# Optimization experiments

Measured on AMD Instinct MI355X. Metric: run time of the kernel, lower is better.

## Reference

```python
import jax, jax.numpy as jnp
import numpy as np

S, B, H, I, E = 512, 2, 1024, 2816, 8  # seq_len, batch, hidden, intermediate, num_local_experts


def setup_inputs() -> dict:
    key = jax.random.key(0)
    ks = jax.random.split(key, 5)
    return {
        "hidden_states": jax.random.normal(ks[0], (S, B, H), dtype=jnp.float32),
        "router_w": jax.random.normal(ks[1], (E, H), dtype=jnp.float32) * 0.02,
        "gate_w": jax.random.normal(ks[2], (E, I, H), dtype=jnp.float32) * 0.02,
        "up_w": jax.random.normal(ks[3], (E, I, H), dtype=jnp.float32) * 0.02,
        "down_w": jax.random.normal(ks[4], (E, H, I), dtype=jnp.float32) * 0.02,
    }


def reference(hidden_states, router_w, gate_w, up_w, down_w):
    # Router: linear hidden -> num_experts, top-1 routing (num_experts_per_tok == 1).
    router_logits = jnp.einsum('sbh,eh->sbe', hidden_states, router_w)  # [S,B,E]
    routing_indices = jnp.argmax(router_logits, axis=-1)  # [S,B], top-1 == argmax
    # NOTE: the source computes routing_weights = sigmoid(top logit) but never
    # applies it in _combine_expert_outputs; we faithfully omit the scaling.

    out = jnp.zeros_like(hidden_states)
    for e in range(E):  # fixed small expert count; masked dense dispatch/combine
        mask = (routing_indices == e)[..., None]  # [S,B,1]
        xe = jnp.where(mask, hidden_states, 0.0)
        g = jnp.einsum('sbh,ih->sbi', xe, gate_w[e])
        u = jnp.einsum('sbh,ih->sbi', xe, up_w[e])
        ye = jnp.einsum('sbi,hi->sbh', jax.nn.silu(g) * u, down_w[e])
        out = out + jnp.where(mask, ye, 0.0)
    return out
```

## Files before the change

kernel.cpp:

```cpp
#include <hip/hip_runtime.h>
#include <math.h>

constexpr int H_ = 1024;
constexpr int I_ = 2816;
constexpr int E_ = 8;
constexpr int T_ = 1024;

typedef __bf16 bf16x8 __attribute__((ext_vector_type(8)));
typedef float f32x4 __attribute__((ext_vector_type(4)));

__device__ __forceinline__ ushort f2bf(float f) {
    uint32_t u = __float_as_uint(f);
    u += 0x7fff + ((u >> 16) & 1);
    return (ushort)(u >> 16);
}
__device__ __forceinline__ uint pack2(float lo, float hi) {
    return (uint)f2bf(lo) | ((uint)f2bf(hi) << 16);
}


__global__ __launch_bounds__(64) void router_kernel(const float* __restrict__ hidden,
                                                    const float* __restrict__ rw,
                                                    int* __restrict__ counts,
                                                    int* __restrict__ tlist,
                                                    ushort* __restrict__ xbf) {
    const int t = blockIdx.x;
    const int lane = threadIdx.x;
    const float* x = hidden + (size_t)t * H_ + lane * 16;
    float4 v[4];
#pragma unroll
    for (int j = 0; j < 4; j++) v[j] = ((const float4*)x)[j];
    uint2* xb = (uint2*)(xbf + (size_t)t * H_ + lane * 16);
#pragma unroll
    for (int j = 0; j < 4; j++) xb[j] = make_uint2(pack2(v[j].x, v[j].y), pack2(v[j].z, v[j].w));
    float acc[E_];
#pragma unroll
    for (int e = 0; e < E_; e++) {
        const float4* r = (const float4*)(rw + e * H_ + lane * 16);
        float a = 0.f;
#pragma unroll
        for (int j = 0; j < 4; j++) {
            float4 rv = r[j];
            a += v[j].x * rv.x + v[j].y * rv.y + v[j].z * rv.z + v[j].w * rv.w;
        }
        acc[e] = a;
    }
#pragma unroll
    for (int e = 0; e < E_; e++) {
#pragma unroll
        for (int off = 32; off >= 1; off >>= 1)
            acc[e] += __shfl_xor(acc[e], off, 64);
    }
    if (lane == 0) {
        int best = 0;
        float bv = acc[0];
#pragma unroll
        for (int e = 1; e < E_; e++) {
            if (acc[e] > bv) { bv = acc[e]; best = e; }
        }
        int pos = atomicAdd(&counts[best], 1);
        tlist[best * T_ + pos] = t;
    }
}

__global__ __launch_bounds__(256, 3) void gateup_kernel(const ushort* __restrict__ xbf,
                                                        const float* __restrict__ gate_w,
                                                        const float* __restrict__ up_w,
                                                        const int* __restrict__ counts,
                                                        const int* __restrict__ tlist,
                                                        ushort* __restrict__ act) {
    const int e  = blockIdx.y;
    const int i0 = blockIdx.x * 32;
    const int cnt = counts[e];
    const int tid = threadIdx.x;

    __shared__ ushort Xs[256 * 72];
    __shared__ ushort Gs[32 * 72];
    __shared__ ushort Us[32 * 72];
    __shared__ int toks[256];

    const int wv = tid >> 6, lane = tid & 63, quad = lane >> 4, l15 = lane & 15;
    const float* gw = gate_w + (size_t)e * I_ * H_ + (size_t)i0 * H_;
    const float* uw = up_w   + (size_t)e * I_ * H_ + (size_t)i0 * H_;

    for (int toff = 0; toff < cnt; toff += 256) {
        __syncthreads();
        {
            int p = toff + tid;
            toks[tid] = (p < cnt) ? tlist[e * T_ + p] : -1;
        }
        __syncthreads();
        int tokr[8];
#pragma unroll
        for (int p = 0; p < 8; p++) tokr[p] = toks[(tid + p * 256) >> 3];

        f32x4 accg[4][2], accu[4][2];
#pragma unroll
        for (int mi = 0; mi < 4; mi++)
#pragma unroll
            for (int nj = 0; nj < 2; nj++) {
                accg[mi][nj] = (f32x4){0.f, 0.f, 0.f, 0.f};
                accu[mi][nj] = (f32x4){0.f, 0.f, 0.f, 0.f};
            }

        uint4 xv[8];
        float4 gv[2], uv[2];
#pragma unroll
        for (int p = 0; p < 8; p++) {
            int idx = tid + p * 256;
            xv[p] = (tokr[p] >= 0)
                ? *(const uint4*)(xbf + (size_t)tokr[p] * H_ + ((idx & 7) << 3))
                : make_uint4(0u, 0u, 0u, 0u);
        }
#pragma unroll
        for (int p = 0; p < 2; p++) {
            int idx = tid + p * 256;
            int row = idx >> 4, c4 = (idx & 15) << 2;
            gv[p] = *(const float4*)(gw + (size_t)row * H_ + c4);
            uv[p] = *(const float4*)(uw + (size_t)row * H_ + c4);
        }

        for (int k0 = 0; k0 < H_; k0 += 64) {
            __syncthreads();
#pragma unroll
            for (int p = 0; p < 8; p++) {
                int idx = tid + p * 256;
                *(uint4*)&Xs[(idx >> 3) * 72 + ((idx & 7) << 3)] = xv[p];
            }
#pragma unroll
            for (int p = 0; p < 2; p++) {
                int idx = tid + p * 256;
                int row = idx >> 4, c4 = (idx & 15) << 2;
                *(uint2*)&Gs[row * 72 + c4] = make_uint2(pack2(gv[p].x, gv[p].y), pack2(gv[p].z, gv[p].w));
                *(uint2*)&Us[row * 72 + c4] = make_uint2(pack2(uv[p].x, uv[p].y), pack2(uv[p].z, uv[p].w));
            }
            if (k0 + 64 < H_) {
                int kn = k0 + 64;
#pragma unroll
                for (int p = 0; p < 8; p++) {
                    int idx = tid + p * 256;
                    xv[p] = (tokr[p] >= 0)
                        ? *(const uint4*)(xbf + (size_t)tokr[p] * H_ + kn + ((idx & 7) << 3))
                        : make_uint4(0u, 0u, 0u, 0u);
                }
#pragma unroll
                for (int p = 0; p < 2; p++) {
                    int idx = tid + p * 256;
                    int row = idx >> 4, c4 = (idx & 15) << 2;
                    gv[p] = *(const float4*)(gw + (size_t)row * H_ + kn + c4);
                    uv[p] = *(const float4*)(uw + (size_t)row * H_ + kn + c4);
                }
            }
            __syncthreads();
#pragma unroll
            for (int kk = 0; kk < 64; kk += 32) {
                const int kb = kk + quad * 8;
                bf16x8 bg[2], bu[2], a[4];
#pragma unroll
                for (int nj = 0; nj < 2; nj++) {
                    bg[nj] = *(const bf16x8*)&Gs[(nj * 16 + l15) * 72 + kb];
                    bu[nj] = *(const bf16x8*)&Us[(nj * 16 + l15) * 72 + kb];
                }
#pragma unroll
                for (int mi = 0; mi < 4; mi++)
                    a[mi] = *(const bf16x8*)&Xs[(wv * 64 + mi * 16 + l15) * 72 + kb];
#pragma unroll
                for (int mi = 0; mi < 4; mi++)
#pragma unroll
                    for (int nj = 0; nj < 2; nj++) {
                        accg[mi][nj] = __builtin_amdgcn_mfma_f32_16x16x32_bf16(a[mi], bg[nj], accg[mi][nj], 0, 0, 0);
                        accu[mi][nj] = __builtin_amdgcn_mfma_f32_16x16x32_bf16(a[mi], bu[nj], accu[mi][nj], 0, 0, 0);
                    }
            }
        }

#pragma unroll
        for (int mi = 0; mi < 4; mi++)
#pragma unroll
            for (int r = 0; r < 4; r++) {
                int tok = toks[wv * 64 + mi * 16 + quad * 4 + r];
                if (tok < 0) continue;
#pragma unroll
                for (int nj = 0; nj < 2; nj++) {
                    float g = accg[mi][nj][r], u = accu[mi][nj][r];
                    float s = g / (1.f + __expf(-g)) * u;
                    act[(size_t)tok * I_ + i0 + nj * 16 + l15] = f2bf(s);
                }
            }
    }
}

__global__ __launch_bounds__(256, 3) void down_kernel(const ushort* __restrict__ act,
                                                      const float* __restrict__ down_w,
                                                      const int* __restrict__ counts,
                                                      const int* __restrict__ tlist,
                                                      float* __restrict__ out) {
    const int e  = blockIdx.y;
    const int h0 = blockIdx.x * 32;
    const int cnt = counts[e];
    const int tid = threadIdx.x;

    __shared__ ushort As[256 * 72];
    __shared__ ushort Ds[32 * 72];
    __shared__ int toks[256];

    const int wv = tid >> 6, lane = tid & 63, quad = lane >> 4, l15 = lane & 15;
    const float* dw = down_w + (size_t)e * H_ * I_ + (size_t)h0 * I_;

    for (int toff = 0; toff < cnt; toff += 256) {
        __syncthreads();
        {
            int p = toff + tid;
            toks[tid] = (p < cnt) ? tlist[e * T_ + p] : -1;
        }
        __syncthreads();
        int tokr[8];
#pragma unroll
        for (int p = 0; p < 8; p++) tokr[p] = toks[(tid + p * 256) >> 3];

        f32x4 acc[4][2];
#pragma unroll
        for (int mi = 0; mi < 4; mi++)
#pragma unroll
            for (int nj = 0; nj < 2; nj++) acc[mi][nj] = (f32x4){0.f, 0.f, 0.f, 0.f};

        uint4 av[8];
        float4 dv[2];
#pragma unroll
        for (int p = 0; p < 8; p++) {
            int idx = tid + p * 256;
            av[p] = (tokr[p] >= 0)
                ? *(const uint4*)(act + (size_t)tokr[p] * I_ + ((idx & 7) << 3))
                : make_uint4(0u, 0u, 0u, 0u);
        }
#pragma unroll
        for (int p = 0; p < 2; p++) {
            int idx = tid + p * 256;
            int row = idx >> 4, c4 = (idx & 15) << 2;
            dv[p] = *(const float4*)(dw + (size_t)row * I_ + c4);
        }

        for (int k0 = 0; k0 < I_; k0 += 64) {
            __syncthreads();
#pragma unroll
            for (int p = 0; p < 8; p++) {
                int idx = tid + p * 256;
                *(uint4*)&As[(idx >> 3) * 72 + ((idx & 7) << 3)] = av[p];
            }
#pragma unroll
            for (int p = 0; p < 2; p++) {
                int idx = tid + p * 256;
                int row = idx >> 4, c4 = (idx & 15) << 2;
                *(uint2*)&Ds[row * 72 + c4] = make_uint2(pack2(dv[p].x, dv[p].y), pack2(dv[p].z, dv[p].w));
            }
            if (k0 + 64 < I_) {
                int kn = k0 + 64;
#pragma unroll
                for (int p = 0; p < 8; p++) {
                    int idx = tid + p * 256;
                    av[p] = (tokr[p] >= 0)
                        ? *(const uint4*)(act + (size_t)tokr[p] * I_ + kn + ((idx & 7) << 3))
                        : make_uint4(0u, 0u, 0u, 0u);
                }
#pragma unroll
                for (int p = 0; p < 2; p++) {
                    int idx = tid + p * 256;
                    int row = idx >> 4, c4 = (idx & 15) << 2;
                    dv[p] = *(const float4*)(dw + (size_t)row * I_ + kn + c4);
                }
            }
            __syncthreads();
#pragma unroll
            for (int kk = 0; kk < 64; kk += 32) {
                const int kb = kk + quad * 8;
                bf16x8 b[2], a[4];
#pragma unroll
                for (int nj = 0; nj < 2; nj++)
                    b[nj] = *(const bf16x8*)&Ds[(nj * 16 + l15) * 72 + kb];
#pragma unroll
                for (int mi = 0; mi < 4; mi++)
                    a[mi] = *(const bf16x8*)&As[(wv * 64 + mi * 16 + l15) * 72 + kb];
#pragma unroll
                for (int mi = 0; mi < 4; mi++)
#pragma unroll
                    for (int nj = 0; nj < 2; nj++)
                        acc[mi][nj] = __builtin_amdgcn_mfma_f32_16x16x32_bf16(a[mi], b[nj], acc[mi][nj], 0, 0, 0);
            }
        }

#pragma unroll
        for (int mi = 0; mi < 4; mi++)
#pragma unroll
            for (int r = 0; r < 4; r++) {
                int tok = toks[wv * 64 + mi * 16 + quad * 4 + r];
                if (tok < 0) continue;
#pragma unroll
                for (int nj = 0; nj < 2; nj++)
                    out[(size_t)tok * H_ + h0 + nj * 16 + l15] = acc[mi][nj][r];
            }
    }
}

extern "C" void kernel_launch(void* const* d_in, const int* in_sizes, int n_in,
                              void* d_out, int out_size, void* d_ws, size_t ws_size,
                              hipStream_t stream) {
    const float* hidden = (const float*)d_in[0];
    const float* rw     = (const float*)d_in[1];
    const float* gate_w = (const float*)d_in[2];
    const float* up_w   = (const float*)d_in[3];
    const float* down_w = (const float*)d_in[4];
    float* out = (float*)d_out;

    int* counts = (int*)d_ws;
    int* tlist  = counts + E_;
    ushort* xbf = (ushort*)(tlist + E_ * T_);
    ushort* act = xbf + (size_t)T_ * H_;

    hipMemsetAsync(counts, 0, E_ * sizeof(int), stream);
    hipLaunchKernelGGL(router_kernel, dim3(T_), dim3(64), 0, stream, hidden, rw, counts, tlist, xbf);
    hipLaunchKernelGGL(gateup_kernel, dim3(I_ / 32, E_), dim3(256), 0, stream,
                       xbf, gate_w, up_w, counts, tlist, act);
    hipLaunchKernelGGL(down_kernel, dim3(H_ / 32, E_), dim3(256), 0, stream,
                       act, down_w, counts, tlist, out);
}
```

Before: 392.7 us.

## Load MFMA operands directly from global into registers, drop LDS staging

Both expert GEMM kernels stop staging token and weight tiles in shared memory. Each lane now loads its MFMA fragment straight from global memory into registers and converts fp32 weights to bf16 in registers. A two-stage register double buffer with an unrolled k loop replaces the __syncthreads-based pipeline, and waves with no tokens now exit early. The down kernel's output tile shrinks to 16 columns with twice as many blocks, and launch bounds drop to 2 blocks per SM. This removes LDS traffic and barriers but loses cross-wave reuse, so each wave re-reads the weights and the gathered activation rows from global or cache.

```diff
diff --git a/kernel.cpp b/kernel.cpp
--- a/kernel.cpp
+++ b/kernel.cpp
@@ -16,6 +16,15 @@
 }
 __device__ __forceinline__ uint pack2(float lo, float hi) {
     return (uint)f2bf(lo) | ((uint)f2bf(hi) << 16);
+}
+__device__ __forceinline__ bf16x8 cvt8(float4 a, float4 b) {
+    union { uint u[4]; bf16x8 v; } r;
+    r.u[0] = pack2(a.x, a.y); r.u[1] = pack2(a.z, a.w);
+    r.u[2] = pack2(b.x, b.y); r.u[3] = pack2(b.z, b.w);
+    return r.v;
+}
+__device__ __forceinline__ bf16x8 as_bf16x8(uint4 v) {
+    union { uint4 u; bf16x8 b; } c; c.u = v; return c.b;
 }
 
 
@@ -63,7 +72,7 @@
     }
 }
 
-__global__ __launch_bounds__(256, 3) void gateup_kernel(const ushort* __restrict__ xbf,
+__global__ __launch_bounds__(256, 2) void gateup_kernel(const ushort* __restrict__ xbf,
                                                         const float* __restrict__ gate_w,
                                                         const float* __restrict__ up_w,
                                                         const int* __restrict__ counts,
@@ -73,26 +82,28 @@
     const int i0 = blockIdx.x * 32;
     const int cnt = counts[e];
     const int tid = threadIdx.x;
-
-    __shared__ ushort Xs[256 * 72];
-    __shared__ ushort Gs[32 * 72];
-    __shared__ ushort Us[32 * 72];
+    const int wv = tid >> 6, lane = tid & 63, quad = lane >> 4, l15 = lane & 15;
+
     __shared__ int toks[256];
 
-    const int wv = tid >> 6, lane = tid & 63, quad = lane >> 4, l15 = lane & 15;
-    const float* gw = gate_w + (size_t)e * I_ * H_ + (size_t)i0 * H_;
-    const float* uw = up_w   + (size_t)e * I_ * H_ + (size_t)i0 * H_;
+    const float* gw0 = gate_w + ((size_t)e * I_ + i0 + l15) * H_ + quad * 8;
+    const float* gw1 = gw0 + (size_t)16 * H_;
+    const float* uw0 = up_w   + ((size_t)e * I_ + i0 + l15) * H_ + quad * 8;
+    const float* uw1 = uw0 + (size_t)16 * H_;
 
     for (int toff = 0; toff < cnt; toff += 256) {
         __syncthreads();
-        {
-            int p = toff + tid;
-            toks[tid] = (p < cnt) ? tlist[e * T_ + p] : -1;
-        }
-        __syncthreads();
-        int tokr[8];
-#pragma unroll
-        for (int p = 0; p < 8; p++) tokr[p] = toks[(tid + p * 256) >> 3];
+        { int p = toff + tid; toks[tid] = (p < cnt) ? tlist[e * T_ + p] : -1; }
+        __syncthreads();
+        if (cnt - toff <= wv * 64) continue;
+
+        int tka[4];
+        const ushort* xa[4];
+#pragma unroll
+        for (int mi = 0; mi < 4; mi++) {
+            tka[mi] = toks[wv * 64 + mi * 16 + l15];
+            xa[mi] = xbf + (size_t)(tka[mi] < 0 ? 0 : tka[mi]) * H_ + quad * 8;
+        }
 
         f32x4 accg[4][2], accu[4][2];
 #pragma unroll
@@ -103,76 +114,49 @@
                 accu[mi][nj] = (f32x4){0.f, 0.f, 0.f, 0.f};
             }
 
-        uint4 xv[8];
-        float4 gv[2], uv[2];
-#pragma unroll
-        for (int p = 0; p < 8; p++) {
-            int idx = tid + p * 256;
-            xv[p] = (tokr[p] >= 0)
-                ? *(const uint4*)(xbf + (size_t)tokr[p] * H_ + ((idx & 7) << 3))
-                : make_uint4(0u, 0u, 0u, 0u);
-        }
-#pragma unroll
-        for (int p = 0; p < 2; p++) {
-            int idx = tid + p * 256;
-            int row = idx >> 4, c4 = (idx & 15) << 2;
-            gv[p] = *(const float4*)(gw + (size_t)row * H_ + c4);
-            uv[p] = *(const float4*)(uw + (size_t)row * H_ + c4);
-        }
-
+        uint4 a0[4], a1[4];
+        float4 g0[2][2], g1[2][2], u0[2][2], u1[2][2];
+
+#define GU_LOAD(A, G, U, kk) do {                                                   \
+        const int k_ = (kk);                                                        \
+        _Pragma("unroll")                                                           \
+        for (int mi = 0; mi < 4; mi++)                                              \
+            A[mi] = (tka[mi] >= 0) ? *(const uint4*)(xa[mi] + k_)                   \
+                                   : make_uint4(0u, 0u, 0u, 0u);                    \
+        G[0][0] = *(const float4*)(gw0 + k_); G[0][1] = *(const float4*)(gw0 + k_ + 4); \
+        G[1][0] = *(const float4*)(gw1 + k_); G[1][1] = *(const float4*)(gw1 + k_ + 4); \
+        U[0][0] = *(const float4*)(uw0 + k_); U[0][1] = *(const float4*)(uw0 + k_ + 4); \
+        U[1][0] = *(const float4*)(uw1 + k_); U[1][1] = *(const float4*)(uw1 + k_ + 4); \
+    } while (0)
+
+#define GU_MFMA(A, G, U) do {                                                       \
+        bf16x8 bg[2], bu[2];                                                        \
+        _Pragma("unroll")                                                           \
+        for (int nj = 0; nj < 2; nj++) {                                            \
+            bg[nj] = cvt8(G[nj][0], G[nj][1]);                                      \
+            bu[nj] = cvt8(U[nj][0], U[nj][1]);                                      \
+        }                                                                           \
+        _Pragma("unroll")                                                           \
+        for (int mi = 0; mi < 4; mi++) {                                            \
+            bf16x8 aa = as_bf16x8(A[mi]);                                           \
+            _Pragma("unroll")                                                       \
+            for (int nj = 0; nj < 2; nj++) {                                        \
+                accg[mi][nj] = __builtin_amdgcn_mfma_f32_16x16x32_bf16(aa, bg[nj], accg[mi][nj], 0, 0, 0); \
+                accu[mi][nj] = __builtin_amdgcn_mfma_f32_16x16x32_bf16(aa, bu[nj], accu[mi][nj], 0, 0, 0); \
+            }                                                                       \
+        }                                                                           \
+    } while (0)
+
+        GU_LOAD(a0, g0, u0, 0);
+#pragma unroll 1
         for (int k0 = 0; k0 < H_; k0 += 64) {
-            __syncthreads();
-#pragma unroll
-            for (int p = 0; p < 8; p++) {
-                int idx = tid + p * 256;
-                *(uint4*)&Xs[(idx >> 3) * 72 + ((idx & 7) << 3)] = xv[p];
-            }
-#pragma unroll
-            for (int p = 0; p < 2; p++) {
-                int idx = tid + p * 256;
-                int row = idx >> 4, c4 = (idx & 15) << 2;
-                *(uint2*)&Gs[row * 72 + c4] = make_uint2(pack2(gv[p].x, gv[p].y), pack2(gv[p].z, gv[p].w));
-                *(uint2*)&Us[row * 72 + c4] = make_uint2(pack2(uv[p].x, uv[p].y), pack2(uv[p].z, uv[p].w));
-            }
-            if (k0 + 64 < H_) {
-                int kn = k0 + 64;
-#pragma unroll
-                for (int p = 0; p < 8; p++) {
-                    int idx = tid + p * 256;
-                    xv[p] = (tokr[p] >= 0)
-                        ? *(const uint4*)(xbf + (size_t)tokr[p] * H_ + kn + ((idx & 7) << 3))
-                        : make_uint4(0u, 0u, 0u, 0u);
-                }
-#pragma unroll
-                for (int p = 0; p < 2; p++) {
-                    int idx = tid + p * 256;
-                    int row = idx >> 4, c4 = (idx & 15) << 2;
-                    gv[p] = *(const float4*)(gw + (size_t)row * H_ + kn + c4);
-                    uv[p] = *(const float4*)(uw + (size_t)row * H_ + kn + c4);
-                }
-            }
-            __syncthreads();
-#pragma unroll
-            for (int kk = 0; kk < 64; kk += 32) {
-                const int kb = kk + quad * 8;
-                bf16x8 bg[2], bu[2], a[4];
-#pragma unroll
-                for (int nj = 0; nj < 2; nj++) {
-                    bg[nj] = *(const bf16x8*)&Gs[(nj * 16 + l15) * 72 + kb];
-                    bu[nj] = *(const bf16x8*)&Us[(nj * 16 + l15) * 72 + kb];
-                }
-#pragma unroll
-                for (int mi = 0; mi < 4; mi++)
-                    a[mi] = *(const bf16x8*)&Xs[(wv * 64 + mi * 16 + l15) * 72 + kb];
-#pragma unroll
-                for (int mi = 0; mi < 4; mi++)
-#pragma unroll
-                    for (int nj = 0; nj < 2; nj++) {
-                        accg[mi][nj] = __builtin_amdgcn_mfma_f32_16x16x32_bf16(a[mi], bg[nj], accg[mi][nj], 0, 0, 0);
-                        accu[mi][nj] = __builtin_amdgcn_mfma_f32_16x16x32_bf16(a[mi], bu[nj], accu[mi][nj], 0, 0, 0);
-                    }
-            }
-        }
+            GU_LOAD(a1, g1, u1, k0 + 32);
+            GU_MFMA(a0, g0, u0);
+            if (k0 + 64 < H_) GU_LOAD(a0, g0, u0, k0 + 64);
+            GU_MFMA(a1, g1, u1);
+        }
+#undef GU_LOAD
+#undef GU_MFMA
 
 #pragma unroll
         for (int mi = 0; mi < 4; mi++)
@@ -190,103 +174,69 @@
     }
 }
 
-__global__ __launch_bounds__(256, 3) void down_kernel(const ushort* __restrict__ act,
+__global__ __launch_bounds__(256, 2) void down_kernel(const ushort* __restrict__ act,
                                                       const float* __restrict__ down_w,
                                                       const int* __restrict__ counts,
                                                       const int* __restrict__ tlist,
                                                       float* __restrict__ out) {
     const int e  = blockIdx.y;
-    const int h0 = blockIdx.x * 32;
+    const int h0 = blockIdx.x * 16;
     const int cnt = counts[e];
     const int tid = threadIdx.x;
-
-    __shared__ ushort As[256 * 72];
-    __shared__ ushort Ds[32 * 72];
+    const int wv = tid >> 6, lane = tid & 63, quad = lane >> 4, l15 = lane & 15;
+
     __shared__ int toks[256];
-
-    const int wv = tid >> 6, lane = tid & 63, quad = lane >> 4, l15 = lane & 15;
-    const float* dw = down_w + (size_t)e * H_ * I_ + (size_t)h0 * I_;
+    const float* dw = down_w + ((size_t)e * H_ + h0 + l15) * I_ + quad * 8;
 
     for (int toff = 0; toff < cnt; toff += 256) {
         __syncthreads();
-        {
-            int p = toff + tid;
-            toks[tid] = (p < cnt) ? tlist[e * T_ + p] : -1;
-        }
-        __syncthreads();
-        int tokr[8];
-#pragma unroll
-        for (int p = 0; p < 8; p++) tokr[p] = toks[(tid + p * 256) >> 3];
-
-        f32x4 acc[4][2];
-#pragma unroll
-        for (int mi = 0; mi < 4; mi++)
-#pragma unroll
-            for (int nj = 0; nj < 2; nj++) acc[mi][nj] = (f32x4){0.f, 0.f, 0.f, 0.f};
-
-        uint4 av[8];
-        float4 dv[2];
-#pragma unroll
-        for (int p = 0; p < 8; p++) {
-            int idx = tid + p * 256;
-            av[p] = (tokr[p] >= 0)
-                ? *(const uint4*)(act + (size_t)tokr[p] * I_ + ((idx & 7) << 3))
-                : make_uint4(0u, 0u, 0u, 0u);
-        }
-#pragma unroll
-        for (int p = 0; p < 2; p++) {
-            int idx = tid + p * 256;
-            int row = idx >> 4, c4 = (idx & 15) << 2;
-            dv[p] = *(const float4*)(dw + (size_t)row * I_ + c4);
-        }
-
+        { int p = toff + tid; toks[tid] = (p < cnt) ? tlist[e * T_ + p] : -1; }
+        __syncthreads();
+        if (cnt - toff <= wv * 64) continue;
+
+        int tka[4];
+        const ushort* xa[4];
+#pragma unroll
+        for (int mi = 0; mi < 4; mi++) {
+            tka[mi] = toks[wv * 64 + mi * 16 + l15];
+            xa[mi] = act + (size_t)(tka[mi] < 0 ? 0 : tka[mi]) * I_ + quad * 8;
+        }
+
+        f32x4 acc[4];
+#pragma unroll
+        for (int mi = 0; mi < 4; mi++) acc[mi] = (f32x4){0.f, 0.f, 0.f, 0.f};
+
+        uint4 a0[4], a1[4];
+        float4 d0[2], d1[2];
+
+#define DN_LOAD(A, D, kk) do {                                                      \
+        const int k_ = (kk);                                                        \
+        _Pragma("unroll")                                                           \
+        for (int mi = 0; mi < 4; mi++)                                              \
+            A[mi] = (tka[mi] >= 0) ? *(const uint4*)(xa[mi] + k_)                   \
+                                   : make_uint4(0u, 0u, 0u, 0u);                    \
+        D[0] = *(const float4*)(dw + k_); D[1] = *(const float4*)(dw + k_ + 4);     \
+    } while (0)
+
+#define DN_MFMA(A, D) do {                                                          \
+        bf16x8 bd = cvt8(D[0], D[1]);                                               \
+        _Pragma("unroll")                                                           \
+        for (int mi = 0; mi < 4; mi++) {                                            \
+            bf16x8 aa = as_bf16x8(A[mi]);                                           \
+            acc[mi] = __builtin_amdgcn_mfma_f32_16x16x32_bf16(aa, bd, acc[mi], 0, 0, 0); \
+        }                                                                           \
+    } while (0)
+
+        DN_LOAD(a0, d0, 0);
+#pragma unroll 1
         for (int k0 = 0; k0 < I_; k0 += 64) {
-            __syncthreads();
-#pragma unroll
-            for (int p = 0; p < 8; p++) {
-                int idx = tid + p * 256;
-                *(uint4*)&As[(idx >> 3) * 72 + ((idx & 7) << 3)] = av[p];
-            }
-#pragma unroll
-            for (int p = 0; p < 2; p++) {
-                int idx = tid + p * 256;
-                int row = idx >> 4, c4 = (idx & 15) << 2;
-                *(uint2*)&Ds[row * 72 + c4] = make_uint2(pack2(dv[p].x, dv[p].y), pack2(dv[p].z, dv[p].w));
-            }
-            if (k0 + 64 < I_) {
-                int kn = k0 + 64;
-#pragma unroll
-                for (int p = 0; p < 8; p++) {
-                    int idx = tid + p * 256;
-                    av[p] = (tokr[p] >= 0)
-                        ? *(const uint4*)(act + (size_t)tokr[p] * I_ + kn + ((idx & 7) << 3))
-                        : make_uint4(0u, 0u, 0u, 0u);
-                }
-#pragma unroll
-                for (int p = 0; p < 2; p++) {
-                    int idx = tid + p * 256;
-                    int row = idx >> 4, c4 = (idx & 15) << 2;
-                    dv[p] = *(const float4*)(dw + (size_t)row * I_ + kn + c4);
-                }
-            }
-            __syncthreads();
-#pragma unroll
-            for (int kk = 0; kk < 64; kk += 32) {
-                const int kb = kk + quad * 8;
-                bf16x8 b[2], a[4];
-#pragma unroll
-                for (int nj = 0; nj < 2; nj++)
-                    b[nj] = *(const bf16x8*)&Ds[(nj * 16 + l15) * 72 + kb];
-#pragma unroll
-                for (int mi = 0; mi < 4; mi++)
-                    a[mi] = *(const bf16x8*)&As[(wv * 64 + mi * 16 + l15) * 72 + kb];
-#pragma unroll
-                for (int mi = 0; mi < 4; mi++)
-#pragma unroll
-                    for (int nj = 0; nj < 2; nj++)
-                        acc[mi][nj] = __builtin_amdgcn_mfma_f32_16x16x32_bf16(a[mi], b[nj], acc[mi][nj], 0, 0, 0);
-            }
-        }
+            DN_LOAD(a1, d1, k0 + 32);
+            DN_MFMA(a0, d0);
+            if (k0 + 64 < I_) DN_LOAD(a0, d0, k0 + 64);
+            DN_MFMA(a1, d1);
+        }
+#undef DN_LOAD
+#undef DN_MFMA
 
 #pragma unroll
         for (int mi = 0; mi < 4; mi++)
@@ -294,9 +244,7 @@
             for (int r = 0; r < 4; r++) {
                 int tok = toks[wv * 64 + mi * 16 + quad * 4 + r];
                 if (tok < 0) continue;
-#pragma unroll
-                for (int nj = 0; nj < 2; nj++)
-                    out[(size_t)tok * H_ + h0 + nj * 16 + l15] = acc[mi][nj][r];
+                out[(size_t)tok * H_ + h0 + l15] = acc[mi][r];
             }
     }
 }
@@ -320,6 +268,6 @@
     hipLaunchKernelGGL(router_kernel, dim3(T_), dim3(64), 0, stream, hidden, rw, counts, tlist, xbf);
     hipLaunchKernelGGL(gateup_kernel, dim3(I_ / 32, E_), dim3(256), 0, stream,
                        xbf, gate_w, up_w, counts, tlist, act);
-    hipLaunchKernelGGL(down_kernel, dim3(H_ / 32, E_), dim3(256), 0, stream,
+    hipLaunchKernelGGL(down_kernel, dim3(H_ / 16, E_), dim3(256), 0, stream,
                        act, down_w, counts, tlist, out);
 }
```

Result: slower. 423.1 us (+7.7%).
